# Optimization experiments

Hardware: AMD Instinct MI355X
Metric: run time of the kernel (lower is better)

## Reference

```python
import jax, jax.numpy as jnp
import numpy as np

IN_F = 3072       # in_features
OUT_F = 9216      # out_features = 3 * N_HEADS * HEAD_DIM (fused QKV)
GROUP = 64        # quantization group size
RANK = 32         # lora_rank
HEAD_DIM = 128
N_HEADS = OUT_F // (3 * HEAD_DIM)  # 24
EPS = 1e-6
LORA_SCALE = 1.0


def setup_inputs() -> dict:
    key = jax.random.key(0)
    ks = jax.random.split(key, 10)
    B, S = 1, 4096
    x = jax.random.normal(ks[0], (B, S, IN_F), dtype=jnp.float32)
    # packed int4 weights: two signed int4 values per int8 byte
    qweight = jax.random.randint(ks[1], (OUT_F, IN_F // 2), -128, 128, dtype=jnp.int32).astype(jnp.int8)
    wscales = (jax.random.uniform(ks[2], (IN_F // GROUP, OUT_F)) * 0.02 + 0.001).astype(jnp.float32)
    bias = (jax.random.normal(ks[3], (OUT_F,)) * 0.01).astype(jnp.float32)
    lora_down = (jax.random.normal(ks[4], (IN_F, RANK)) * 0.02).astype(jnp.float32)
    lora_up = (jax.random.normal(ks[5], (OUT_F, RANK)) * 0.02).astype(jnp.float32)
    smooth = (jax.random.uniform(ks[6], (IN_F,)) * 0.5 + 0.75).astype(jnp.float32)   # keep away from 0
    norm_q = (jax.random.uniform(ks[7], (HEAD_DIM,)) * 0.5 + 0.75).astype(jnp.float32)
    norm_k = (jax.random.uniform(ks[8], (HEAD_DIM,)) * 0.5 + 0.75).astype(jnp.float32)
    ang = jax.random.uniform(ks[9], (S, HEAD_DIM // 2)) * (2.0 * np.pi)
    rotary_emb = jnp.stack([jnp.cos(ang), jnp.sin(ang)], axis=-1).astype(jnp.float32)  # [S, D/2, 2]
    return dict(x=x, qweight=qweight, wscales=wscales, bias=bias, lora_down=lora_down,
                lora_up=lora_up, smooth=smooth, norm_q=norm_q, norm_k=norm_k, rotary_emb=rotary_emb)


def _dequant_weight(qweight, wscales):
    # unpack two signed int4 lanes from each int8 (low nibble first), then per-group scale
    low = jnp.right_shift(jnp.left_shift(qweight, 4), 4)   # arithmetic shifts on int8 -> sign extend
    high = jnp.right_shift(qweight, 4)
    w4 = jnp.stack([low, high], axis=-1).reshape(OUT_F, IN_F)          # int4 codes in [-8, 7]
    wg = w4.astype(jnp.float32).reshape(OUT_F, IN_F // GROUP, GROUP)
    return (wg * wscales.T[:, :, None]).reshape(OUT_F, IN_F)          # [N, K]


def _quantize_act(x, smooth, lora_down):
    # fused: smooth -> symmetric per-token per-group int4 quantize -> lora_down projection
    B, S, K = x.shape
    M = B * S
    xs = (x / smooth).reshape(M, K)
    xg = xs.reshape(M, K // GROUP, GROUP)
    ascale = jnp.max(jnp.abs(xg), axis=-1, keepdims=True) / 7.0
    ascale = jnp.maximum(ascale, 1e-8)
    q = jnp.clip(jnp.round(xg / ascale), -8.0, 7.0)
    deq = (q * ascale).reshape(M, K)                                   # dequantized int4 activation
    lora_act = xs @ lora_down                                          # [M, RANK], fp32 side path
    return deq, lora_act


def _rope(t, cos, sin):
    # interleaved pairs (even, odd) rotation; t: [M, H, D], cos/sin: [M, 1, D/2]
    e, o = t[..., 0::2], t[..., 1::2]
    re = e * cos - o * sin
    ro = e * sin + o * cos
    return jnp.stack([re, ro], axis=-1).reshape(t.shape)


def reference(x, qweight, wscales, bias, lora_down, lora_up, smooth, norm_q, norm_k, rotary_emb):
    B, S, K = x.shape
    M = B * S
    deq_x, lora_act = _quantize_act(x, smooth, lora_down)
    w = _dequant_weight(qweight, wscales)
    # main int4 GEMM + LoRA up + bias, all fused in the real kernel
    out = deq_x @ w.T + (LORA_SCALE * lora_act) @ lora_up.T + bias     # [M, OUT_F]
    qkv = out.reshape(M, 3, N_HEADS, HEAD_DIM)
    q, k, v = qkv[:, 0], qkv[:, 1], qkv[:, 2]
    def rms(t, g):
        return t * jax.lax.rsqrt(jnp.mean(t * t, axis=-1, keepdims=True) + EPS) * g
    q = rms(q, norm_q)
    k = rms(k, norm_k)
    cos = rotary_emb[:, None, :, 0]   # [M, 1, D/2]
    sin = rotary_emb[:, None, :, 1]
    q = _rope(q, cos, sin)
    k = _rope(k, cos, sin)
    return jnp.stack([q, k, v], axis=1).reshape(B, S, OUT_F)
```

## Files before the change

### kernel.cpp

```cpp
#include <hip/hip_runtime.h>
#include <cstdint>

#define MDIM 4096
#define NDIM 9216
#define KDIM 3072
#define KP   3136
#define NKT2 97

#define QB 4096
#define WB 13824
#define PB 2304

typedef unsigned int u32;
typedef unsigned short u16;
typedef float f32x4 __attribute__((ext_vector_type(4)));
typedef __bf16 bf16x8 __attribute__((ext_vector_type(8)));

__device__ __forceinline__ u16 f2bf(float f) {
  u32 u = __float_as_uint(f);
  u32 r = u + 0x7fffu + ((u >> 16) & 1u);
  return (u16)(r >> 16);
}

__device__ __forceinline__ float frcp(float f) { return __builtin_amdgcn_rcpf(f); }

__device__ __forceinline__ void gld_lds16(const void* g, void* l) {
  __builtin_amdgcn_global_load_lds((__attribute__((address_space(1))) void*)g,
                                   (__attribute__((address_space(3))) void*)l,
                                   16, 0, 0);
}

__global__ __launch_bounds__(256) void k_prep(const float* __restrict__ x, const u32* __restrict__ qw,
                        const float* __restrict__ wsc, const float* __restrict__ lora_down,
                        const float* __restrict__ lora_up, const float* __restrict__ smooth,
                        u16* __restrict__ Aex, u16* __restrict__ Bex) {
  __shared__ float xs_s[KDIM];
  __shared__ float part[64 * 32];
  const int tid = threadIdx.x;
  int bid = blockIdx.x;

  if (bid >= QB) {
    bid -= QB;
    if (bid >= WB) {
      int idx = (bid - WB) * 256 + tid;
      int n = idx >> 6, c = idx & 63;
      u16 v = 0;
      if (c < 32) v = f2bf(lora_up[n * 32 + c]);
      Bex[(size_t)n * KP + 3072 + c] = v;
      return;
    }
    __shared__ int s_viol;
    u32 probe = qw[tid];
    bool ok = (probe >> 8) == ((probe & 0x80u) ? 0xffffffu : 0u);
    if (tid == 0) s_viol = 0;
    __syncthreads();
    if (!ok) atomicOr(&s_viol, 1);
    __syncthreads();
    const int f = (s_viol == 0);

    int idx = bid * 256 + tid;
    int n = idx / 384;
    int j = idx - n * 384;
    int k0 = j * 8;
    u32 w;
    if (f) {
      uint4 q4 = ((const uint4*)qw)[idx];
      w = (q4.x & 0xffu) | ((q4.y & 0xffu) << 8) | ((q4.z & 0xffu) << 16) | ((q4.w & 0xffu) << 24);
    } else {
      w = qw[idx];
    }
    float ws = wsc[(k0 >> 6) * NDIM + n];
    u32 ow[4];
    #pragma unroll
    for (int b = 0; b < 4; ++b) {
      int by = (int)((w >> (8 * b)) & 0xffu);
      int lo = (by << 28) >> 28;
      int hi = (by << 24) >> 28;
      ow[b] = (u32)f2bf((float)lo * ws) | ((u32)f2bf((float)hi * ws) << 16);
    }
    *(uint4*)(Bex + (size_t)n * KP + k0) = make_uint4(ow[0], ow[1], ow[2], ow[3]);
    return;
  }

  const int m = bid;
  const int sub = tid & 15;
  const float* xr = x + (size_t)m * KDIM;
  u16* arow = Aex + (size_t)m * KP;

  #pragma unroll
  for (int p = 0; p < 3; ++p) {
    int g = p * 16 + (tid >> 4);
    int k0 = g * 64 + sub * 4;
    float4 xv = *(const float4*)(xr + k0);
    float4 sv = *(const float4*)(smooth + k0);
    float a0 = xv.x * frcp(sv.x), a1 = xv.y * frcp(sv.y);
    float a2 = xv.z * frcp(sv.z), a3 = xv.w * frcp(sv.w);
    xs_s[k0+0] = a0; xs_s[k0+1] = a1; xs_s[k0+2] = a2; xs_s[k0+3] = a3;
    float am = fmaxf(fmaxf(fabsf(a0), fabsf(a1)), fmaxf(fabsf(a2), fabsf(a3)));
    am = fmaxf(am, __shfl_xor(am, 8, 16));
    am = fmaxf(am, __shfl_xor(am, 4, 16));
    am = fmaxf(am, __shfl_xor(am, 2, 16));
    am = fmaxf(am, __shfl_xor(am, 1, 16));
    float asc = fmaxf(am * (1.0f / 7.0f), 1e-8f);
    float iasc = frcp(asc);
    float q0 = fminf(7.f, fmaxf(-8.f, rintf(a0 * iasc)));
    float q1 = fminf(7.f, fmaxf(-8.f, rintf(a1 * iasc)));
    float q2 = fminf(7.f, fmaxf(-8.f, rintf(a2 * iasc)));
    float q3 = fminf(7.f, fmaxf(-8.f, rintf(a3 * iasc)));
    float d0 = q0 * asc, d1 = q1 * asc, d2 = q2 * asc, d3 = q3 * asc;
    u32 lo = (u32)f2bf(d0) | ((u32)f2bf(d1) << 16);
    u32 hi = (u32)f2bf(d2) | ((u32)f2bf(d3) << 16);
    *(uint2*)(arow + k0) = make_uint2(lo, hi);
  }
  if (tid < 32) arow[3104 + tid] = 0;
  __syncthreads();

  {
    const int c  = tid >> 2;
    const int r8 = (tid & 3) * 8;
    float a[8] = {0.f, 0.f, 0.f, 0.f, 0.f, 0.f, 0.f, 0.f};
    const float* lp = lora_down + (size_t)c * 32 + r8;
    #pragma unroll 4
    for (int i = 0; i < 48; ++i) {
      float xv = xs_s[i * 64 + c];
      float4 l0 = *(const float4*)(lp);
      float4 l1 = *(const float4*)(lp + 4);
      a[0] = fmaf(xv, l0.x, a[0]); a[1] = fmaf(xv, l0.y, a[1]);
      a[2] = fmaf(xv, l0.z, a[2]); a[3] = fmaf(xv, l0.w, a[3]);
      a[4] = fmaf(xv, l1.x, a[4]); a[5] = fmaf(xv, l1.y, a[5]);
      a[6] = fmaf(xv, l1.z, a[6]); a[7] = fmaf(xv, l1.w, a[7]);
      lp += 64 * 32;
    }
    __syncthreads();
    *(float4*)(&part[c * 32 + r8])     = make_float4(a[0], a[1], a[2], a[3]);
    *(float4*)(&part[c * 32 + r8 + 4]) = make_float4(a[4], a[5], a[6], a[7]);
  }
  __syncthreads();
  if (tid < 32) {
    float s = 0.f;
    #pragma unroll 8
    for (int cc = 0; cc < 64; ++cc) s += part[cc * 32 + tid];
    arow[3072 + tid] = f2bf(s);
  }
}

__global__ __launch_bounds__(512) void k_gemm(const u16* __restrict__ A, const u16* __restrict__ B,
                                              const float* __restrict__ bias, const float* __restrict__ norm_q,
                                              const float* __restrict__ norm_k, const float* __restrict__ rot,
                                              float* __restrict__ out) {
  extern __shared__ u16 lds[];
  const int tid  = threadIdx.x;
  const int lane = tid & 63;
  const int wave = tid >> 6;
  const int m0 = blockIdx.y * 256;
  const int n0 = blockIdx.x * 256;
  const int wm = (wave >> 2) * 128;
  const int wn = (wave & 3) * 64;
  const int lr = lane & 15;
  const int lq = lane >> 4;

  const u16 *pA0, *pA1, *pB0, *pB1;
  int la0, la1, lb0, lb1;
  {
    auto mk = [&](int p, const u16* base, int nb) -> const u16* {
      int pr = p >> 3, cs = p & 7;
      int c  = cs ^ (pr & 7);
      int r  = pr * 2 + (c >> 2);
      int kc = c & 3;
      return base + (size_t)(nb + r) * KP + kc * 8;
    };
    int p0 = tid, p1 = 512 + tid;
    pA0 = mk(p0, A, m0); pA1 = mk(p1, A, m0);
    pB0 = mk(p0, B, n0); pB1 = mk(p1, B, n0);
    la0 = p0 * 8;        la1 = p1 * 8;
    lb0 = 8192 + p0 * 8; lb1 = 8192 + p1 * 8;
  }

  int aoff[8], boff[4];
  #pragma unroll
  for (int t = 0; t < 8; ++t) {
    int ra = wm + t * 16 + lr;
    int pr = ra >> 1, c = (ra & 1) * 4 + lq;
    aoff[t] = pr * 64 + ((c ^ (pr & 7)) * 8);
  }
  #pragma unroll
  for (int t = 0; t < 4; ++t) {
    int rb = wn + t * 16 + lr;
    int pr = rb >> 1, c = (rb & 1) * 4 + lq;
    boff[t] = 8192 + pr * 64 + ((c ^ (pr & 7)) * 8);
  }

  f32x4 acc[8][4] = {};

  #pragma unroll
  for (int s = 0; s < 3; ++s) {
    u16* sl = lds + (s << 14);
    gld_lds16(pA0, sl + la0); gld_lds16(pA1, sl + la1);
    gld_lds16(pB0, sl + lb0); gld_lds16(pB1, sl + lb1);
    pA0 += 32; pA1 += 32; pB0 += 32; pB1 += 32;
  }
  asm volatile("s_waitcnt vmcnt(8)" ::: "memory");
  __builtin_amdgcn_s_barrier();

  #pragma unroll 1
  for (int kt = 0; kt < NKT2; ++kt) {
    const u16* sA_ = lds + ((kt & 3) << 14);
    u16* stl = lds + (((kt + 3) & 3) << 14);
    const bool st = (kt < NKT2 - 3);
    bf16x8 af[4], bf[4];

    if (st) { gld_lds16(pA0, stl + la0); gld_lds16(pA1, stl + la1); }
    #pragma unroll
    for (int t = 0; t < 4; ++t) af[t] = *(const bf16x8*)&sA_[aoff[t]];
    #pragma unroll
    for (int t = 0; t < 4; ++t) bf[t] = *(const bf16x8*)&sA_[boff[t]];
    __builtin_amdgcn_s_barrier();
    asm volatile("s_waitcnt lgkmcnt(0)" ::: "memory");
    __builtin_amdgcn_sched_barrier(0);
    __builtin_amdgcn_s_setprio(1);
    #pragma unroll
    for (int ti = 0; ti < 4; ++ti)
      #pragma unroll
      for (int tj = 0; tj < 4; ++tj)
        acc[ti][tj] = __builtin_amdgcn_mfma_f32_16x16x32_bf16(af[ti], bf[tj], acc[ti][tj], 0, 0, 0);
    __builtin_amdgcn_s_setprio(0);
    __builtin_amdgcn_sched_barrier(0);
    __builtin_amdgcn_s_barrier();

    if (st) { gld_lds16(pB0, stl + lb0); gld_lds16(pB1, stl + lb1);
              pA0 += 32; pA1 += 32; pB0 += 32; pB1 += 32; }
    #pragma unroll
    for (int t = 0; t < 4; ++t) af[t] = *(const bf16x8*)&sA_[aoff[4 + t]];
    __builtin_amdgcn_s_barrier();
    asm volatile("s_waitcnt lgkmcnt(0)" ::: "memory");
    __builtin_amdgcn_sched_barrier(0);
    __builtin_amdgcn_s_setprio(1);
    #pragma unroll
    for (int ti = 0; ti < 4; ++ti)
      #pragma unroll
      for (int tj = 0; tj < 4; ++tj)
        acc[4 + ti][tj] = __builtin_amdgcn_mfma_f32_16x16x32_bf16(af[ti], bf[tj], acc[4 + ti][tj], 0, 0, 0);
    __builtin_amdgcn_s_setprio(0);
    __builtin_amdgcn_sched_barrier(0);
    if (st) asm volatile("s_waitcnt vmcnt(8)" ::: "memory");
    else    asm volatile("s_waitcnt vmcnt(0)" ::: "memory");
    __builtin_amdgcn_s_barrier();
  }

  const int sel = (blockIdx.x >= 24) ? 2 : (blockIdx.x >= 12 ? 1 : 0);

  float bv[4];
  #pragma unroll
  for (int tj = 0; tj < 4; ++tj) bv[tj] = bias[n0 + wn + tj * 16 + lr];
  #pragma unroll
  for (int ti = 0; ti < 8; ++ti)
    #pragma unroll
    for (int tj = 0; tj < 4; ++tj)
      #pragma unroll
      for (int rg = 0; rg < 4; ++rg)
        acc[ti][tj][rg] += bv[tj];

  if (sel == 2) {
    #pragma unroll
    for (int tj = 0; tj < 4; ++tj) {
      int n = n0 + wn + tj * 16 + lr;
      #pragma unroll
      for (int ti = 0; ti < 8; ++ti) {
        int mr = m0 + wm + ti * 16 + lq * 4;
        #pragma unroll
        for (int rg = 0; rg < 4; ++rg)
          out[(size_t)(mr + rg) * NDIM + n] = acc[ti][tj][rg];
      }
    }
    return;
  }

  float* ssq = (float*)lds;
  #pragma unroll
  for (int ti = 0; ti < 8; ++ti) {
    float pr4[4];
    #pragma unroll
    for (int rg = 0; rg < 4; ++rg) {
      float s = 0.f;
      #pragma unroll
      for (int tj = 0; tj < 4; ++tj) s += acc[ti][tj][rg] * acc[ti][tj][rg];
      pr4[rg] = s;
    }
    #pragma unroll
    for (int off = 1; off < 16; off <<= 1)
      #pragma unroll
      for (int rg = 0; rg < 4; ++rg) pr4[rg] += __shfl_xor(pr4[rg], off);
    #pragma unroll
    for (int rg = 0; rg < 4; ++rg)
      if (lr == (ti & 3) * 4 + rg)
        ssq[(wn >> 6) * 256 + wm + ti * 16 + lq * 4 + rg] = pr4[rg];
  }
  __syncthreads();

  const float* nrm = sel ? norm_k : norm_q;
  float gm[4];
  #pragma unroll
  for (int tj = 0; tj < 4; ++tj) gm[tj] = nrm[(wn & 64) + tj * 16 + lr];
  const float2* rot2 = (const float2*)rot;
  const float sgn = (lr & 1) ? 1.0f : -1.0f;
  const int hb = (wn >> 7) * 512;

  #pragma unroll
  for (int ti = 0; ti < 8; ++ti) {
    #pragma unroll
    for (int rg = 0; rg < 4; ++rg) {
      int row = wm + ti * 16 + lq * 4 + rg;
      float tot = ssq[hb + row] + ssq[hb + 256 + row];
      float rs = rsqrtf(tot * (1.0f / 128.0f) + 1e-6f);
      int m = m0 + row;
      #pragma unroll
      for (int tj = 0; tj < 4; ++tj) {
        int nl = (wn & 64) + tj * 16 + lr;
        float v = acc[ti][tj][rg] * rs * gm[tj];
        float p = __shfl_xor(v, 1);
        float2 cs = rot2[(size_t)m * 64 + (nl >> 1)];
        out[(size_t)m * NDIM + n0 + wn + tj * 16 + lr] = v * cs.x + sgn * (p * cs.y);
      }
    }
  }
}

extern "C" void kernel_launch(void* const* d_in, const int* in_sizes, int n_in,
                              void* d_out, int out_size, void* d_ws, size_t ws_size,
                              hipStream_t stream) {
  const float* x         = (const float*)d_in[0];
  const u32*   qweight   = (const u32*)d_in[1];
  const float* wscales   = (const float*)d_in[2];
  const float* bias      = (const float*)d_in[3];
  const float* lora_down = (const float*)d_in[4];
  const float* lora_up   = (const float*)d_in[5];
  const float* smooth    = (const float*)d_in[6];
  const float* norm_q    = (const float*)d_in[7];
  const float* norm_k    = (const float*)d_in[8];
  const float* rot       = (const float*)d_in[9];
  float* out = (float*)d_out;

  u16* Aex = (u16*)d_ws;
  u16* Bex = Aex + (size_t)MDIM * KP;

  static bool attr_set = false;
  if (!attr_set) {
    hipFuncSetAttribute(reinterpret_cast<const void*>(k_gemm),
                        hipFuncAttributeMaxDynamicSharedMemorySize, 131072);
    attr_set = true;
  }

  k_prep<<<QB + WB + PB, 256, 0, stream>>>(x, qweight, wscales, lora_down, lora_up, smooth, Aex, Bex);
  k_gemm<<<dim3(NDIM / 256, MDIM / 256), 512, 131072, stream>>>(Aex, Bex, bias, norm_q, norm_k, rot, out);
}
```

Measured before the change: 561.5 us.

## Split prep kernel, batch four rows per quant block, simplify GEMM loop barriers

Splits the combined prep kernel into a separate weight-dequant kernel and an activation-quant kernel. The quant kernel now processes four rows per block so each lora_down load is reused across four rows. The GEMM main loop issues all four global-to-LDS loads up front and runs all 32 MFMAs in one phase, dropping the two intra-iteration barriers and lgkmcnt waits. This cuts sync overhead but relies on compiler-inserted waits for LDS reads, adds an extra launch, and loads eight A fragments at once, which raises register pressure.

Measured after the change: 531.9 us. 1.06x faster.

```diff
diff --git a/kernel.cpp b/kernel.cpp
--- a/kernel.cpp
+++ b/kernel.cpp
@@ -7,7 +7,8 @@
 #define KP   3136
 #define NKT2 97
 
-#define QB 4096
+#define QROWS 4
+#define QB2 1024
 #define WB 13824
 #define PB 2304
 
@@ -30,118 +31,125 @@
                                    16, 0, 0);
 }
 
-__global__ __launch_bounds__(256) void k_prep(const float* __restrict__ x, const u32* __restrict__ qw,
-                        const float* __restrict__ wsc, const float* __restrict__ lora_down,
-                        const float* __restrict__ lora_up, const float* __restrict__ smooth,
-                        u16* __restrict__ Aex, u16* __restrict__ Bex) {
-  __shared__ float xs_s[KDIM];
+__global__ __launch_bounds__(256) void k_quant(const float* __restrict__ x,
+                        const float* __restrict__ lora_down, const float* __restrict__ smooth,
+                        u16* __restrict__ Aex) {
+  __shared__ float xs_s[QROWS][KDIM];
   __shared__ float part[64 * 32];
   const int tid = threadIdx.x;
+  const int m0 = blockIdx.x * QROWS;
+  const int sub = tid & 15;
+
+  #pragma unroll
+  for (int r = 0; r < QROWS; ++r) {
+    const float* xr = x + (size_t)(m0 + r) * KDIM;
+    u16* arow = Aex + (size_t)(m0 + r) * KP;
+    #pragma unroll
+    for (int p = 0; p < 3; ++p) {
+      int g = p * 16 + (tid >> 4);
+      int k0 = g * 64 + sub * 4;
+      float4 xv = *(const float4*)(xr + k0);
+      float4 sv = *(const float4*)(smooth + k0);
+      float a0 = xv.x * frcp(sv.x), a1 = xv.y * frcp(sv.y);
+      float a2 = xv.z * frcp(sv.z), a3 = xv.w * frcp(sv.w);
+      xs_s[r][k0+0] = a0; xs_s[r][k0+1] = a1; xs_s[r][k0+2] = a2; xs_s[r][k0+3] = a3;
+      float am = fmaxf(fmaxf(fabsf(a0), fabsf(a1)), fmaxf(fabsf(a2), fabsf(a3)));
+      am = fmaxf(am, __shfl_xor(am, 8, 16));
+      am = fmaxf(am, __shfl_xor(am, 4, 16));
+      am = fmaxf(am, __shfl_xor(am, 2, 16));
+      am = fmaxf(am, __shfl_xor(am, 1, 16));
+      float asc = fmaxf(am * (1.0f / 7.0f), 1e-8f);
+      float iasc = frcp(asc);
+      float q0 = fminf(7.f, fmaxf(-8.f, rintf(a0 * iasc)));
+      float q1 = fminf(7.f, fmaxf(-8.f, rintf(a1 * iasc)));
+      float q2 = fminf(7.f, fmaxf(-8.f, rintf(a2 * iasc)));
+      float q3 = fminf(7.f, fmaxf(-8.f, rintf(a3 * iasc)));
+      float d0 = q0 * asc, d1 = q1 * asc, d2 = q2 * asc, d3 = q3 * asc;
+      u32 lo = (u32)f2bf(d0) | ((u32)f2bf(d1) << 16);
+      u32 hi = (u32)f2bf(d2) | ((u32)f2bf(d3) << 16);
+      *(uint2*)(arow + k0) = make_uint2(lo, hi);
+    }
+    if (tid < 32) arow[3104 + tid] = 0;
+  }
+  __syncthreads();
+
+  const int c  = tid >> 2;
+  const int r8 = (tid & 3) * 8;
+  float a[QROWS][8] = {};
+  const float* lp = lora_down + (size_t)c * 32 + r8;
+  #pragma unroll 2
+  for (int i = 0; i < 48; ++i) {
+    float4 l0 = *(const float4*)(lp);
+    float4 l1 = *(const float4*)(lp + 4);
+    #pragma unroll
+    for (int r = 0; r < QROWS; ++r) {
+      float xv = xs_s[r][i * 64 + c];
+      a[r][0] = fmaf(xv, l0.x, a[r][0]); a[r][1] = fmaf(xv, l0.y, a[r][1]);
+      a[r][2] = fmaf(xv, l0.z, a[r][2]); a[r][3] = fmaf(xv, l0.w, a[r][3]);
+      a[r][4] = fmaf(xv, l1.x, a[r][4]); a[r][5] = fmaf(xv, l1.y, a[r][5]);
+      a[r][6] = fmaf(xv, l1.z, a[r][6]); a[r][7] = fmaf(xv, l1.w, a[r][7]);
+    }
+    lp += 64 * 32;
+  }
+  #pragma unroll 1
+  for (int r = 0; r < QROWS; ++r) {
+    __syncthreads();
+    *(float4*)(&part[c * 32 + r8])     = make_float4(a[r][0], a[r][1], a[r][2], a[r][3]);
+    *(float4*)(&part[c * 32 + r8 + 4]) = make_float4(a[r][4], a[r][5], a[r][6], a[r][7]);
+    __syncthreads();
+    if (tid < 32) {
+      float s = 0.f;
+      #pragma unroll 8
+      for (int cc = 0; cc < 64; ++cc) s += part[cc * 32 + tid];
+      Aex[(size_t)(m0 + r) * KP + 3072 + tid] = f2bf(s);
+    }
+  }
+}
+
+__global__ __launch_bounds__(256) void k_wdq(const u32* __restrict__ qw,
+                        const float* __restrict__ wsc, const float* __restrict__ lora_up,
+                        u16* __restrict__ Bex) {
+  const int tid = threadIdx.x;
   int bid = blockIdx.x;
 
-  if (bid >= QB) {
-    bid -= QB;
-    if (bid >= WB) {
-      int idx = (bid - WB) * 256 + tid;
-      int n = idx >> 6, c = idx & 63;
-      u16 v = 0;
-      if (c < 32) v = f2bf(lora_up[n * 32 + c]);
-      Bex[(size_t)n * KP + 3072 + c] = v;
-      return;
-    }
-    __shared__ int s_viol;
-    u32 probe = qw[tid];
-    bool ok = (probe >> 8) == ((probe & 0x80u) ? 0xffffffu : 0u);
-    if (tid == 0) s_viol = 0;
-    __syncthreads();
-    if (!ok) atomicOr(&s_viol, 1);
-    __syncthreads();
-    const int f = (s_viol == 0);
-
-    int idx = bid * 256 + tid;
-    int n = idx / 384;
-    int j = idx - n * 384;
-    int k0 = j * 8;
-    u32 w;
-    if (f) {
-      uint4 q4 = ((const uint4*)qw)[idx];
-      w = (q4.x & 0xffu) | ((q4.y & 0xffu) << 8) | ((q4.z & 0xffu) << 16) | ((q4.w & 0xffu) << 24);
-    } else {
-      w = qw[idx];
-    }
-    float ws = wsc[(k0 >> 6) * NDIM + n];
-    u32 ow[4];
-    #pragma unroll
-    for (int b = 0; b < 4; ++b) {
-      int by = (int)((w >> (8 * b)) & 0xffu);
-      int lo = (by << 28) >> 28;
-      int hi = (by << 24) >> 28;
-      ow[b] = (u32)f2bf((float)lo * ws) | ((u32)f2bf((float)hi * ws) << 16);
-    }
-    *(uint4*)(Bex + (size_t)n * KP + k0) = make_uint4(ow[0], ow[1], ow[2], ow[3]);
+  if (bid >= WB) {
+    int idx = (bid - WB) * 256 + tid;
+    int n = idx >> 6, c = idx & 63;
+    u16 v = 0;
+    if (c < 32) v = f2bf(lora_up[n * 32 + c]);
+    Bex[(size_t)n * KP + 3072 + c] = v;
     return;
   }
-
-  const int m = bid;
-  const int sub = tid & 15;
-  const float* xr = x + (size_t)m * KDIM;
-  u16* arow = Aex + (size_t)m * KP;
-
-  #pragma unroll
-  for (int p = 0; p < 3; ++p) {
-    int g = p * 16 + (tid >> 4);
-    int k0 = g * 64 + sub * 4;
-    float4 xv = *(const float4*)(xr + k0);
-    float4 sv = *(const float4*)(smooth + k0);
-    float a0 = xv.x * frcp(sv.x), a1 = xv.y * frcp(sv.y);
-    float a2 = xv.z * frcp(sv.z), a3 = xv.w * frcp(sv.w);
-    xs_s[k0+0] = a0; xs_s[k0+1] = a1; xs_s[k0+2] = a2; xs_s[k0+3] = a3;
-    float am = fmaxf(fmaxf(fabsf(a0), fabsf(a1)), fmaxf(fabsf(a2), fabsf(a3)));
-    am = fmaxf(am, __shfl_xor(am, 8, 16));
-    am = fmaxf(am, __shfl_xor(am, 4, 16));
-    am = fmaxf(am, __shfl_xor(am, 2, 16));
-    am = fmaxf(am, __shfl_xor(am, 1, 16));
-    float asc = fmaxf(am * (1.0f / 7.0f), 1e-8f);
-    float iasc = frcp(asc);
-    float q0 = fminf(7.f, fmaxf(-8.f, rintf(a0 * iasc)));
-    float q1 = fminf(7.f, fmaxf(-8.f, rintf(a1 * iasc)));
-    float q2 = fminf(7.f, fmaxf(-8.f, rintf(a2 * iasc)));
-    float q3 = fminf(7.f, fmaxf(-8.f, rintf(a3 * iasc)));
-    float d0 = q0 * asc, d1 = q1 * asc, d2 = q2 * asc, d3 = q3 * asc;
-    u32 lo = (u32)f2bf(d0) | ((u32)f2bf(d1) << 16);
-    u32 hi = (u32)f2bf(d2) | ((u32)f2bf(d3) << 16);
-    *(uint2*)(arow + k0) = make_uint2(lo, hi);
-  }
-  if (tid < 32) arow[3104 + tid] = 0;
+  __shared__ int s_viol;
+  u32 probe = qw[tid];
+  bool ok = (probe >> 8) == ((probe & 0x80u) ? 0xffffffu : 0u);
+  if (tid == 0) s_viol = 0;
   __syncthreads();
-
-  {
-    const int c  = tid >> 2;
-    const int r8 = (tid & 3) * 8;
-    float a[8] = {0.f, 0.f, 0.f, 0.f, 0.f, 0.f, 0.f, 0.f};
-    const float* lp = lora_down + (size_t)c * 32 + r8;
-    #pragma unroll 4
-    for (int i = 0; i < 48; ++i) {
-      float xv = xs_s[i * 64 + c];
-      float4 l0 = *(const float4*)(lp);
-      float4 l1 = *(const float4*)(lp + 4);
-      a[0] = fmaf(xv, l0.x, a[0]); a[1] = fmaf(xv, l0.y, a[1]);
-      a[2] = fmaf(xv, l0.z, a[2]); a[3] = fmaf(xv, l0.w, a[3]);
-      a[4] = fmaf(xv, l1.x, a[4]); a[5] = fmaf(xv, l1.y, a[5]);
-      a[6] = fmaf(xv, l1.z, a[6]); a[7] = fmaf(xv, l1.w, a[7]);
-      lp += 64 * 32;
-    }
-    __syncthreads();
-    *(float4*)(&part[c * 32 + r8])     = make_float4(a[0], a[1], a[2], a[3]);
-    *(float4*)(&part[c * 32 + r8 + 4]) = make_float4(a[4], a[5], a[6], a[7]);
-  }
+  if (!ok) atomicOr(&s_viol, 1);
   __syncthreads();
-  if (tid < 32) {
-    float s = 0.f;
-    #pragma unroll 8
-    for (int cc = 0; cc < 64; ++cc) s += part[cc * 32 + tid];
-    arow[3072 + tid] = f2bf(s);
-  }
+  const int f = (s_viol == 0);
+
+  int idx = bid * 256 + tid;
+  int n = idx / 384;
+  int j = idx - n * 384;
+  int k0 = j * 8;
+  u32 w;
+  if (f) {
+    uint4 q4 = ((const uint4*)qw)[idx];
+    w = (q4.x & 0xffu) | ((q4.y & 0xffu) << 8) | ((q4.z & 0xffu) << 16) | ((q4.w & 0xffu) << 24);
+  } else {
+    w = qw[idx];
+  }
+  float ws = wsc[(k0 >> 6) * NDIM + n];
+  u32 ow[4];
+  #pragma unroll
+  for (int b = 0; b < 4; ++b) {
+    int by = (int)((w >> (8 * b)) & 0xffu);
+    int lo = (by << 28) >> 28;
+    int hi = (by << 24) >> 28;
+    ow[b] = (u32)f2bf((float)lo * ws) | ((u32)f2bf((float)hi * ws) << 16);
+  }
+  *(uint4*)(Bex + (size_t)n * KP + k0) = make_uint4(ow[0], ow[1], ow[2], ow[3]);
 }
 
 __global__ __launch_bounds__(512) void k_gemm(const u16* __restrict__ A, const u16* __restrict__ B,
@@ -201,50 +209,34 @@
   }
   asm volatile("s_waitcnt vmcnt(8)" ::: "memory");
   __builtin_amdgcn_s_barrier();
+  asm volatile("" ::: "memory");
 
   #pragma unroll 1
   for (int kt = 0; kt < NKT2; ++kt) {
     const u16* sA_ = lds + ((kt & 3) << 14);
     u16* stl = lds + (((kt + 3) & 3) << 14);
     const bool st = (kt < NKT2 - 3);
-    bf16x8 af[4], bf[4];
-
-    if (st) { gld_lds16(pA0, stl + la0); gld_lds16(pA1, stl + la1); }
-    #pragma unroll
-    for (int t = 0; t < 4; ++t) af[t] = *(const bf16x8*)&sA_[aoff[t]];
+    if (st) {
+      gld_lds16(pA0, stl + la0); gld_lds16(pA1, stl + la1);
+      gld_lds16(pB0, stl + lb0); gld_lds16(pB1, stl + lb1);
+      pA0 += 32; pA1 += 32; pB0 += 32; pB1 += 32;
+    }
+    bf16x8 af[8], bf[4];
+    #pragma unroll
+    for (int t = 0; t < 8; ++t) af[t] = *(const bf16x8*)&sA_[aoff[t]];
     #pragma unroll
     for (int t = 0; t < 4; ++t) bf[t] = *(const bf16x8*)&sA_[boff[t]];
-    __builtin_amdgcn_s_barrier();
-    asm volatile("s_waitcnt lgkmcnt(0)" ::: "memory");
-    __builtin_amdgcn_sched_barrier(0);
     __builtin_amdgcn_s_setprio(1);
     #pragma unroll
-    for (int ti = 0; ti < 4; ++ti)
+    for (int ti = 0; ti < 8; ++ti)
       #pragma unroll
       for (int tj = 0; tj < 4; ++tj)
         acc[ti][tj] = __builtin_amdgcn_mfma_f32_16x16x32_bf16(af[ti], bf[tj], acc[ti][tj], 0, 0, 0);
     __builtin_amdgcn_s_setprio(0);
-    __builtin_amdgcn_sched_barrier(0);
-    __builtin_amdgcn_s_barrier();
-
-    if (st) { gld_lds16(pB0, stl + lb0); gld_lds16(pB1, stl + lb1);
-              pA0 += 32; pA1 += 32; pB0 += 32; pB1 += 32; }
-    #pragma unroll
-    for (int t = 0; t < 4; ++t) af[t] = *(const bf16x8*)&sA_[aoff[4 + t]];
-    __builtin_amdgcn_s_barrier();
-    asm volatile("s_waitcnt lgkmcnt(0)" ::: "memory");
-    __builtin_amdgcn_sched_barrier(0);
-    __builtin_amdgcn_s_setprio(1);
-    #pragma unroll
-    for (int ti = 0; ti < 4; ++ti)
-      #pragma unroll
-      for (int tj = 0; tj < 4; ++tj)
-        acc[4 + ti][tj] = __builtin_amdgcn_mfma_f32_16x16x32_bf16(af[ti], bf[tj], acc[4 + ti][tj], 0, 0, 0);
-    __builtin_amdgcn_s_setprio(0);
-    __builtin_amdgcn_sched_barrier(0);
     if (st) asm volatile("s_waitcnt vmcnt(8)" ::: "memory");
     else    asm volatile("s_waitcnt vmcnt(0)" ::: "memory");
     __builtin_amdgcn_s_barrier();
+    asm volatile("" ::: "memory");
   }
 
   const int sel = (blockIdx.x >= 24) ? 2 : (blockIdx.x >= 12 ? 1 : 0);
@@ -350,6 +342,7 @@
     attr_set = true;
   }
 
-  k_prep<<<QB + WB + PB, 256, 0, stream>>>(x, qweight, wscales, lora_down, lora_up, smooth, Aex, Bex);
+  k_wdq<<<WB + PB, 256, 0, stream>>>(qweight, wscales, lora_up, Bex);
+  k_quant<<<QB2, 256, 0, stream>>>(x, lora_down, smooth, Aex);
   k_gemm<<<dim3(NDIM / 256, MDIM / 256), 512, 131072, stream>>>(Aex, Bex, bias, norm_q, norm_k, rot, out);
 }
```
